# Optimization experiments

Hardware: AMD Instinct MI355X
Metric: run time of the kernel (lower is better)

Reference implementation:

```python
import jax, jax.numpy as jnp
import numpy as np
import math

N = 50000        # nodes
DEG = 16         # regular out-degree -> E = N*DEG edges, grouped by source node
B = 64           # graphs in batch
F = 128          # num_node_features
H = 128          # nhid == enhid
RATIO = 0.5      # edge_ratio
NUM_CONVS = 3
E = N * DEG


def setup_inputs() -> dict:
    key = jax.random.key(0)
    ks = jax.random.split(key, 18)
    s = 0.05
    x = jax.random.normal(ks[0], (N, F), jnp.float32)
    edge_src = jnp.repeat(jnp.arange(N, dtype=jnp.int32), DEG)          # sorted by src
    edge_dst = jax.random.randint(ks[1], (E,), 0, N, jnp.int32)
    batch = ((jnp.arange(N) * B) // N).astype(jnp.int32)                 # sorted graph ids
    edge_attr = jnp.ones((E, 1), jnp.float32)                            # edge_attr=None branch
    inp = {"x": x, "edge_attr": edge_attr, "edge_src": edge_src,
           "edge_dst": edge_dst, "batch": batch}
    # GCNConv weights: [F->H, H->H, H->H]
    inp["W_gcn0"] = jax.random.normal(ks[2], (F, H), jnp.float32) * s
    inp["b_gcn0"] = jnp.zeros((H,), jnp.float32)
    inp["W_gcn1"] = jax.random.normal(ks[3], (H, H), jnp.float32) * s
    inp["b_gcn1"] = jnp.zeros((H,), jnp.float32)
    inp["W_gcn2"] = jax.random.normal(ks[4], (H, H), jnp.float32) * s
    inp["b_gcn2"] = jnp.zeros((H,), jnp.float32)
    # EGNN edge convs: [1->H, H->H]
    inp["W_eg0"] = jax.random.normal(ks[5], (1, H), jnp.float32) * s
    inp["b_eg0"] = jnp.zeros((H,), jnp.float32)
    inp["W_eg1"] = jax.random.normal(ks[6], (H, H), jnp.float32) * s
    inp["b_eg1"] = jnp.zeros((H,), jnp.float32)
    # score convs: [H->1, H->1]
    inp["W_sc0"] = jax.random.normal(ks[7], (H, 1), jnp.float32) * s
    inp["b_sc0"] = jnp.zeros((1,), jnp.float32)
    inp["W_sc1"] = jax.random.normal(ks[8], (H, 1), jnp.float32) * s
    inp["b_sc1"] = jnp.zeros((1,), jnp.float32)
    return inp


def _gcn(x, src, dst, ew, W, b):
    # PyG GCNConv: add self-loops (weight 1), symmetric deg normalization, aggregate at dst.
    n = x.shape[0]
    loop = jnp.arange(n, dtype=src.dtype)
    src2 = jnp.concatenate([src, loop])
    dst2 = jnp.concatenate([dst, loop])
    ew2 = jnp.concatenate([ew, jnp.ones((n,), ew.dtype)])
    deg = jax.ops.segment_sum(ew2, dst2, n)
    dinv = jnp.where(deg > 0, jax.lax.rsqrt(jnp.maximum(deg, 1e-12)), 0.0)
    norm = dinv[src2] * dinv[dst2] * ew2                                  # [E+n]
    msg = (x @ W)[src2] * norm[:, None]                                    # gather + scale
    return jax.ops.segment_sum(msg, dst2, n) + b                           # scatter-add


def _egnn(e, src, W, b):
    # Edge conv: scatter edge features to their source node, gather back, linear map.
    agg = jax.ops.segment_sum(e, src, N)
    return agg[src] @ W + b


def _pool(h, batch):
    gmax = jax.ops.segment_max(h, batch, B)
    gsum = jax.ops.segment_sum(h, batch, B)
    cnt = jax.ops.segment_sum(jnp.ones((h.shape[0],), h.dtype), batch, B)
    gmean = gsum / cnt[:, None]
    return jnp.concatenate([gmax, gmean, gsum], axis=1)                    # [B, 3H]


def reference(x, edge_attr, edge_src, edge_dst, batch,
              W_gcn0, b_gcn0, W_gcn1, b_gcn1, W_gcn2, b_gcn2,
              W_eg0, b_eg0, W_eg1, b_eg1, W_sc0, b_sc0, W_sc1, b_sc1):
    gW = [W_gcn0, W_gcn1, W_gcn2]
    gb = [b_gcn0, b_gcn1, b_gcn2]
    eW = [W_eg0, W_eg1]
    eb = [b_eg0, b_eg1]
    sW = [W_sc0, W_sc1]
    sb = [b_sc0, b_sc1]
    src, dst = edge_src, edge_dst
    deg = DEG
    ew = jnp.ones((src.shape[0],), jnp.float32)
    h = x
    ea = edge_attr
    xs = jnp.zeros((B, 3 * H), jnp.float32)
    for i in range(NUM_CONVS):
        h = jax.nn.relu(_gcn(h, src, dst, ew, gW[i], gb[i]))
        if i < NUM_CONVS - 1:
            ea = jax.nn.relu(_egnn(ea, src, eW[i], eb[i]))
            score = jnp.tanh(_egnn(ea, src, sW[i], sb[i])[:, 0])           # [E_cur]
            k = math.ceil(RATIO * deg)                                      # per-src-node top-k
            vals, idx = jax.lax.top_k(score.reshape(N, deg), k)             # [N,k]
            dst = jnp.take_along_axis(dst.reshape(N, deg), idx, axis=1).reshape(-1)
            flat = (jnp.arange(N)[:, None] * deg + idx).reshape(-1)
            ea = ea[flat]
            src = jnp.repeat(jnp.arange(N, dtype=src.dtype), k)
            ew = jnp.clip(vals.reshape(-1), 0.0, 1.0)
            deg = k
        xs = xs + _pool(h, batch)
    return xs
```

## Files before the change

kernel.cpp:

```cpp
#include <hip/hip_runtime.h>
#include <math.h>

#define NNODES 50000
#define DEGREE 16
#define NGRAPH 64
#define CAP 64
#define LDA 136
#define NXCD 8
#define XRANGE (NNODES / NXCD)
#define NTILE 782
#define ACHUNK 784
#define BCAP 192

typedef unsigned short u16;
typedef unsigned int u32;
typedef unsigned long long u64;
using short8 = __attribute__((ext_vector_type(8))) short;
using f32x4  = __attribute__((ext_vector_type(4))) float;
using fv4    = __attribute__((ext_vector_type(4))) float;

__device__ __forceinline__ u16 f2bf(float f) {
  union { float f; u32 u; } v; v.f = f;
  u32 u = v.u;
  return (u16)((u + 0x7FFFu + ((u >> 16) & 1u)) >> 16);
}
__device__ __forceinline__ float2 bf2x2(u32 u) {
  union { u32 u; float f; } lo, hi;
  lo.u = (u & 0xFFFFu) << 16; hi.u = u & 0xFFFF0000u;
  return make_float2(lo.f, hi.f);
}
__device__ __forceinline__ u32 pack2(float x, float y) {
  return (u32)f2bf(x) | ((u32)f2bf(y) << 16);
}
__device__ __forceinline__ int lowerb(const int* b, int n, int v) {
  int lo = 0, hi = n;
  while (lo < hi) { int m = (lo + hi) >> 1; if (b[m] < v) lo = m + 1; else hi = m; }
  return lo;
}

__device__ __forceinline__ void cons8(uint4 v, float w, float* acc) {
  float2 p;
  p = bf2x2(v.x); acc[0] = fmaf(w, p.x, acc[0]); acc[1] = fmaf(w, p.y, acc[1]);
  p = bf2x2(v.y); acc[2] = fmaf(w, p.x, acc[2]); acc[3] = fmaf(w, p.y, acc[3]);
  p = bf2x2(v.z); acc[4] = fmaf(w, p.x, acc[4]); acc[5] = fmaf(w, p.y, acc[5]);
  p = bf2x2(v.w); acc[6] = fmaf(w, p.x, acc[6]); acc[7] = fmaf(w, p.y, acc[7]);
}
__device__ __forceinline__ void consP(uint4 v, float* mx, float* sm) {
  float2 p;
  p = bf2x2(v.x);
  mx[0] = fmaxf(mx[0], p.x); sm[0] += p.x; mx[1] = fmaxf(mx[1], p.y); sm[1] += p.y;
  p = bf2x2(v.y);
  mx[2] = fmaxf(mx[2], p.x); sm[2] += p.x; mx[3] = fmaxf(mx[3], p.y); sm[3] += p.y;
  p = bf2x2(v.z);
  mx[4] = fmaxf(mx[4], p.x); sm[4] += p.x; mx[5] = fmaxf(mx[5], p.y); sm[5] += p.y;
  p = bf2x2(v.w);
  mx[6] = fmaxf(mx[6], p.x); sm[6] += p.x; mx[7] = fmaxf(mx[7], p.y); sm[7] += p.y;
}

__global__ __launch_bounds__(256) void k_init(
    const float* __restrict__ eattr,
    const float* __restrict__ weg, const float* __restrict__ beg,
    const float* __restrict__ wsc, const float* __restrict__ bsc,
    const float* __restrict__ W0, const float* __restrict__ W1,
    const float* __restrict__ W2, const float* __restrict__ W3,
    float* __restrict__ ew1, float* __restrict__ agg0, u16* __restrict__ Wt,
    const int* __restrict__ edst, int* __restrict__ cnt,
    int* __restrict__ slots, int2* __restrict__ stag, int* __restrict__ scnt) {
  __shared__ int2 lbuf[NXCD * BCAP];
  __shared__ int lcnt[NXCD];
  int b = blockIdx.x, t = threadIdx.x;
  if (b < 196) {
    int i = b * 256 + t;
    if (i < NNODES) {
      const fv4* p = reinterpret_cast<const fv4*>(eattr + (size_t)i * DEGREE);
      float s = 0.f;
#pragma unroll
      for (int j = 0; j < 4; ++j) {
        fv4 w = __builtin_nontemporal_load(&p[j]);
        s += w.x + w.y + w.z + w.w;
      }
      agg0[i] = s;
      float sc = 0.f;
      for (int k = 0; k < 128; ++k) {
        float e = fmaxf(fmaf(s, weg[k], beg[k]), 0.f);
        sc = fmaf(e, wsc[k], sc);
      }
      float v1 = tanhf(fmaf(16.f, sc, bsc[0]));
      ew1[i] = fminf(fmaxf(v1, 0.f), 1.f);
    }
  } else if (b < 452) {
    int idx = (b - 196) * 256 + t;
    int which = idx >> 14, r = idx & 16383;
    int k = r >> 7, n = r & 127;
    const float* W = which == 0 ? W0 : which == 1 ? W1 : which == 2 ? W2 : W3;
    Wt[which * 16384 + n * 128 + k] = f2bf(W[k * 128 + n]);
  } else {
    int b2 = b - 452;
    if (t < NXCD) lcnt[t] = 0;
    __syncthreads();
    int e0 = b2 * ACHUNK;
    for (int k = 0; k < ACHUNK; k += 256) {
      int idx = k + t;
      int e = e0 + idx;
      if (idx < ACHUNK && e < NNODES * DEGREE) {
        int d = edst[e];
        u32 r = (u32)d / (u32)XRANGE;
        int pos = atomicAdd(&lcnt[r], 1);
        if (pos < BCAP) {
          lbuf[r * BCAP + pos] = make_int2(e, d);
        } else {
          int gp = atomicAdd(&cnt[d], 1);
          if (gp < CAP) slots[(size_t)d * CAP + gp] = e;
        }
      }
    }
    __syncthreads();
    for (int idx = t; idx < NXCD * BCAP; idx += 256) {
      int r = idx / BCAP, i = idx - r * BCAP;
      if (i < min(lcnt[r], BCAP))
        stag[((size_t)r * 1024 + b2) * BCAP + i] = lbuf[idx];
    }
    if (t < NXCD) scnt[t * 1024 + b2] = min(lcnt[t], BCAP);
  }
}

__global__ __launch_bounds__(256) void k_gemmF(
    int nFill, const int2* __restrict__ stag, const int* __restrict__ scnt,
    int* __restrict__ cnt, int* __restrict__ slots,
    int nGemm, const u16* __restrict__ A, const float* __restrict__ Af32,
    const u16* __restrict__ WtA, u16* __restrict__ outA,
    int nEg, const float* __restrict__ agg0, const float* __restrict__ weg,
    const float* __restrict__ beg, const u16* __restrict__ WtE,
    const float* __restrict__ beE, const float* __restrict__ wsc1,
    const float* __restrict__ bs1, float* __restrict__ ewOut) {
  __shared__ u16 Bs[128 * LDA];
  __shared__ u16 As[64 * LDA];
  int b = blockIdx.x, t = threadIdx.x;
  if (b < nFill) {
    int r = b & (NXCD - 1), sub = b >> 3;
    for (int q = 0; q < 8; ++q) {
      int sb = sub * 8 + q;
      int c = scnt[r * 1024 + sb];
      const int2* src = &stag[((size_t)r * 1024 + sb) * BCAP];
      for (int i = t; i < c; i += 256) {
        int2 v = src[i];
        int pos = atomicAdd(&cnt[v.y], 1);
        if (pos < CAP) slots[(size_t)v.y * CAP + pos] = v.x;
      }
    }
    return;
  }
  int bb = b - nFill;
  int eg = (bb >= nGemm);
  const u16* Wsrc = eg ? WtE : WtA;
  for (int i = t; i < 2048; i += 256) {
    int r = i >> 4, c = (i & 15) << 3;
    *reinterpret_cast<uint4*>(&Bs[r * LDA + c]) =
        *reinterpret_cast<const uint4*>(&Wsrc[r * 128 + c]);
  }
  int m0 = (eg ? (bb - nGemm) : bb) * 64;
  if (eg) {
    for (int idx = t; idx < 64 * 128; idx += 256) {
      int r = idx >> 7, k = idx & 127;
      int row = m0 + r;
      float a = (row < NNODES) ? agg0[row] : 0.f;
      float v = 8.f * fmaxf(fmaf(a, weg[k], beg[k]), 0.f);
      As[r * LDA + k] = f2bf(v);
    }
  } else if (Af32) {
    for (int i = t; i < 1024; i += 256) {
      int r = i >> 4, c = (i & 15) << 3;
      int row = m0 + r;
      uint4 o = make_uint4(0u, 0u, 0u, 0u);
      if (row < NNODES) {
        const fv4* px = reinterpret_cast<const fv4*>(Af32 + (size_t)row * 128 + c);
        fv4 v0 = __builtin_nontemporal_load(&px[0]);
        fv4 v1 = __builtin_nontemporal_load(&px[1]);
        o.x = pack2(v0.x, v0.y); o.y = pack2(v0.z, v0.w);
        o.z = pack2(v1.x, v1.y); o.w = pack2(v1.z, v1.w);
      }
      *reinterpret_cast<uint4*>(&As[r * LDA + c]) = o;
    }
  } else {
    for (int i = t; i < 1024; i += 256) {
      int r = i >> 4, c = (i & 15) << 3;
      int row = m0 + r;
      uint4 v = make_uint4(0u, 0u, 0u, 0u);
      if (row < NNODES) v = *reinterpret_cast<const uint4*>(&A[(size_t)row * 128 + c]);
      *reinterpret_cast<uint4*>(&As[r * LDA + c]) = v;
    }
  }
  __syncthreads();
  int wave = t >> 6, lane = t & 63;
  int lm = lane & 15, quad = lane >> 4;
  f32x4 z = {0.f, 0.f, 0.f, 0.f};
  f32x4 acc[8];
#pragma unroll
  for (int n = 0; n < 8; ++n) acc[n] = z;
  const u16* arow = &As[(wave * 16 + lm) * LDA + quad * 8];
#pragma unroll
  for (int kc = 0; kc < 4; ++kc) {
    short8 af = *reinterpret_cast<const short8*>(arow + kc * 32);
#pragma unroll
    for (int n = 0; n < 8; ++n) {
      short8 bf = *reinterpret_cast<const short8*>(
          &Bs[(n * 16 + lm) * LDA + kc * 32 + quad * 8]);
      acc[n] = __builtin_amdgcn_mfma_f32_16x16x32_bf16(af, bf, acc[n], 0, 0, 0);
    }
  }
  if (!eg) {
#pragma unroll
    for (int n = 0; n < 8; ++n) {
      int col = n * 16 + lm;
#pragma unroll
      for (int r = 0; r < 4; ++r) {
        int row = m0 + wave * 16 + quad * 4 + r;
        if (row < NNODES) outA[(size_t)row * 128 + col] = f2bf(acc[n][r]);
      }
    }
  } else {
    float s0 = 0.f, s1 = 0.f, s2 = 0.f, s3 = 0.f;
#pragma unroll
    for (int n = 0; n < 8; ++n) {
      int col = n * 16 + lm;
      float bb2 = beE[col], wv = wsc1[col];
      s0 = fmaf(fmaxf(acc[n][0] + bb2, 0.f), wv, s0);
      s1 = fmaf(fmaxf(acc[n][1] + bb2, 0.f), wv, s1);
      s2 = fmaf(fmaxf(acc[n][2] + bb2, 0.f), wv, s2);
      s3 = fmaf(fmaxf(acc[n][3] + bb2, 0.f), wv, s3);
    }
#pragma unroll
    for (int m = 8; m >= 1; m >>= 1) {
      s0 += __shfl_xor(s0, m, 64);
      s1 += __shfl_xor(s1, m, 64);
      s2 += __shfl_xor(s2, m, 64);
      s3 += __shfl_xor(s3, m, 64);
    }
    if (lm == 0) {
      float bsv = bs1[0];
      float sv[4] = {s0, s1, s2, s3};
#pragma unroll
      for (int r = 0; r < 4; ++r) {
        int row = m0 + wave * 16 + quad * 4 + r;
        if (row < NNODES) {
          float v = tanhf(fmaf(8.f, sv[r], bsv));
          ewOut[row] = fminf(fmaxf(v, 0.f), 1.f);
        }
      }
    }
  }
}

template <int MODE>
__global__ __launch_bounds__(256) void k_agg(
    int nAgg, const u16* __restrict__ xwb, const int* __restrict__ cnt,
    const int* __restrict__ slots, const float* __restrict__ wsrc,
    const float* __restrict__ dinv, const float* __restrict__ bias,
    u16* __restrict__ hout,
    const u16* __restrict__ hpool, const int* __restrict__ batch,
    float* __restrict__ out,
    const float* __restrict__ ew1g, float* __restrict__ dv1,
    float* __restrict__ ws1,
    const float* __restrict__ ew2g, float* __restrict__ dv2,
    float* __restrict__ ws2) {
  constexpr int keep = (MODE == 0) ? 16 : (MODE == 1) ? 8 : 4;
  constexpr bool L0 = (MODE == 0);
  constexpr int poolAdd = (MODE >= 2);
  __shared__ float P[1024];
  int b = blockIdx.x, t = threadIdx.x;
  int lane = t & 63;
  int q = lane >> 4, li = lane & 15;
  if (b < nAgg) {
    int n = (b * 256 + t) >> 6;
    if (n >= NNODES) return;
    int c = min(cnt[n], CAP);
    u32 e = 0;
    if (lane < c) e = (u32)slots[(size_t)n * CAP + lane];
    if (L0) {
      u32 j = e & 15u; int srcn = (int)(e >> 4);
      float e1 = 0.f, e2 = 0.f;
      if (lane < c && j < 8u) {
        e1 = ew1g[srcn];
        if (j < 4u) e2 = ew2g[srcn];
      }
#pragma unroll
      for (int m = 32; m >= 1; m >>= 1) {
        e1 += __shfl_xor(e1, m, 64);
        e2 += __shfl_xor(e2, m, 64);
      }
      if (lane == 0) {
        float d1 = rsqrtf(1.0f + e1), d2 = rsqrtf(1.0f + e2);
        dv1[n] = d1; ws1[n] = d1 * ew1g[n];
        dv2[n] = d2; ws2[n] = d2 * ew2g[n];
      }
    }
    int kc; u32 ce;
    if (keep < 16) {
      bool valid = (lane < c) && ((e & 15u) < (u32)keep);
      u64 mask = __ballot(valid);
      kc = (int)__popcll(mask);
      u64 lt = ((u64)1 << lane) - 1;
      int pos = valid ? (int)__popcll(mask & lt) : 63 - (int)__popcll((~mask) & lt);
      ce = (u32)__builtin_amdgcn_ds_permute(pos << 2, (int)e);
    } else { kc = c; ce = e; }
    int sl = 0; float wl = 0.f;
    if (lane < kc) {
      sl = (int)(ce >> 4);
      wl = L0 ? rsqrtf(1.0f + (float)min(cnt[sl], CAP)) : wsrc[sl];
    }
    const uint4* b4 = reinterpret_cast<const uint4*>(xwb);
    uint4 selfv = b4[n * 16 + li];
    float acc[8] = {0.f, 0.f, 0.f, 0.f, 0.f, 0.f, 0.f, 0.f};
    for (int i = 0; i < kc; i += 16) {
      int r0 = i + q, r1 = i + 4 + q, r2 = i + 8 + q, r3 = i + 12 + q;
      int s0 = __shfl(sl, r0, 64); float w0 = __shfl(wl, r0, 64);
      int s1 = __shfl(sl, r1, 64); float w1 = __shfl(wl, r1, 64);
      int s2 = __shfl(sl, r2, 64); float w2 = __shfl(wl, r2, 64);
      int s3 = __shfl(sl, r3, 64); float w3 = __shfl(wl, r3, 64);
      if (r0 >= kc) { s0 = n; w0 = 0.f; }
      if (r1 >= kc) { s1 = n; w1 = 0.f; }
      if (r2 >= kc) { s2 = n; w2 = 0.f; }
      if (r3 >= kc) { s3 = n; w3 = 0.f; }
      uint4 v0 = b4[s0 * 16 + li];
      uint4 v1 = selfv, v2 = selfv, v3 = selfv;
      if (i + 4 < kc)  v1 = b4[s1 * 16 + li];
      if (i + 8 < kc)  v2 = b4[s2 * 16 + li];
      if (i + 12 < kc) v3 = b4[s3 * 16 + li];
      cons8(v0, w0, acc);
      cons8(v1, w1, acc);
      cons8(v2, w2, acc);
      cons8(v3, w3, acc);
    }
#pragma unroll
    for (int k = 0; k < 8; ++k) {
      acc[k] += __shfl_xor(acc[k], 16, 64);
      acc[k] += __shfl_xor(acc[k], 32, 64);
    }
    float di = L0 ? rsqrtf(1.0f + (float)c) : dinv[n];
    float dd = di * di;
    const f32x4* bp = reinterpret_cast<const f32x4*>(bias);
    f32x4 bv0 = bp[li * 2], bv1 = bp[li * 2 + 1];
    float2 p0 = bf2x2(selfv.x), p1 = bf2x2(selfv.y),
           p2 = bf2x2(selfv.z), p3 = bf2x2(selfv.w);
    float r0 = fmaxf(fmaf(di, acc[0], fmaf(dd, p0.x, bv0.x)), 0.f);
    float r1 = fmaxf(fmaf(di, acc[1], fmaf(dd, p0.y, bv0.y)), 0.f);
    float r2 = fmaxf(fmaf(di, acc[2], fmaf(dd, p1.x, bv0.z)), 0.f);
    float r3 = fmaxf(fmaf(di, acc[3], fmaf(dd, p1.y, bv0.w)), 0.f);
    float r4 = fmaxf(fmaf(di, acc[4], fmaf(dd, p2.x, bv1.x)), 0.f);
    float r5 = fmaxf(fmaf(di, acc[5], fmaf(dd, p2.y, bv1.y)), 0.f);
    float r6 = fmaxf(fmaf(di, acc[6], fmaf(dd, p3.x, bv1.z)), 0.f);
    float r7 = fmaxf(fmaf(di, acc[7], fmaf(dd, p3.y, bv1.w)), 0.f);
    if (q == 0) {
      uint4 o;
      o.x = pack2(r0, r1); o.y = pack2(r2, r3);
      o.z = pack2(r4, r5); o.w = pack2(r6, r7);
      reinterpret_cast<uint4*>(hout + (size_t)n * 128)[li] = o;
    }
  } else {
    int g = b - nAgg;
    int wv = t >> 6;
    int lo = lowerb(batch, NNODES, g);
    int hi = lowerb(batch, NNODES, g + 1);
    const uint4* hb4 = reinterpret_cast<const uint4*>(hpool);
    float mx[8] = {0.f, 0.f, 0.f, 0.f, 0.f, 0.f, 0.f, 0.f};
    float sm[8] = {0.f, 0.f, 0.f, 0.f, 0.f, 0.f, 0.f, 0.f};
    int n = lo + wv * 4 + q;
    for (; n + 48 < hi; n += 64) {
      uint4 v0 = hb4[(size_t)n * 16 + li];
      uint4 v1 = hb4[(size_t)(n + 16) * 16 + li];
      uint4 v2 = hb4[(size_t)(n + 32) * 16 + li];
      uint4 v3 = hb4[(size_t)(n + 48) * 16 + li];
      consP(v0, mx, sm); consP(v1, mx, sm);
      consP(v2, mx, sm); consP(v3, mx, sm);
    }
    for (; n < hi; n += 16) {
      uint4 v = hb4[(size_t)n * 16 + li];
      consP(v, mx, sm);
    }
#pragma unroll
    for (int k = 0; k < 8; ++k) {
      mx[k] = fmaxf(mx[k], __shfl_xor(mx[k], 16, 64));
      mx[k] = fmaxf(mx[k], __shfl_xor(mx[k], 32, 64));
      sm[k] += __shfl_xor(sm[k], 16, 64);
      sm[k] += __shfl_xor(sm[k], 32, 64);
    }
    if (q == 0) {
#pragma unroll
      for (int k = 0; k < 8; ++k) {
        P[(wv * 16 + li) * 16 + k] = mx[k];
        P[(wv * 16 + li) * 16 + 8 + k] = sm[k];
      }
    }
    __syncthreads();
    if (t < 128) {
      int li2 = t >> 3, k = t & 7;
      int o0 = li2 * 16 + k, o1 = o0 + 8;
      float m = fmaxf(fmaxf(P[o0], P[256 + o0]),
                      fmaxf(P[512 + o0], P[768 + o0]));
      float s = P[o1] + P[256 + o1] + P[512 + o1] + P[768 + o1];
      float cf = (float)(hi - lo);
      int col = li2 * 8 + k;
      float* og = out + g * 384;
      if (poolAdd) {
        og[col] += m; og[128 + col] += s / cf; og[256 + col] += s;
      } else {
        og[col] = m;  og[128 + col] = s / cf;  og[256 + col] = s;
      }
    }
  }
}

extern "C" void kernel_launch(void* const* d_in, const int* in_sizes, int n_in,
                              void* d_out, int out_size, void* d_ws, size_t ws_size,
                              hipStream_t stream) {
  const float* x     = (const float*)d_in[0];
  const float* eattr = (const float*)d_in[1];
  const int*   edst  = (const int*)d_in[3];
  const int*   batch = (const int*)d_in[4];
  const float* Wg0 = (const float*)d_in[5];  const float* bg0 = (const float*)d_in[6];
  const float* Wg1 = (const float*)d_in[7];  const float* bg1 = (const float*)d_in[8];
  const float* Wg2 = (const float*)d_in[9];  const float* bg2 = (const float*)d_in[10];
  const float* We0 = (const float*)d_in[11]; const float* be0 = (const float*)d_in[12];
  const float* We1 = (const float*)d_in[13]; const float* be1 = (const float*)d_in[14];
  const float* Ws0 = (const float*)d_in[15]; const float* bs0 = (const float*)d_in[16];
  const float* Ws1 = (const float*)d_in[17]; const float* bs1 = (const float*)d_in[18];
  float* out = (float*)d_out;

  char* ws = (char*)d_ws;
  const size_t NBH = (size_t)NNODES * 128 * 2;
  size_t off = 0;
  auto alloc = [&](size_t bytes) { void* p = ws + off; off = (off + bytes + 255) & ~(size_t)255; return p; };
  u16*   XWb   = (u16*)alloc(NBH);
  u16*   Hb0   = (u16*)alloc(NBH);
  u16*   Hb1   = (u16*)alloc(NBH);
  u16*   Hb2   = (u16*)alloc(NBH);
  u16*   Wtb   = (u16*)alloc(4 * 128 * 128 * 2);
  int*   slots = (int*)alloc((size_t)NNODES * CAP * 4);
  int*   cnt   = (int*)alloc((size_t)NNODES * 4);
  int2*  stag  = (int2*)alloc((size_t)NXCD * 1024 * BCAP * 8);
  int*   scnt  = (int*)alloc((size_t)NXCD * 1024 * 4);
  float* agg0  = (float*)alloc((size_t)NNODES * 4);
  float* ew1   = (float*)alloc((size_t)NNODES * 4);
  float* ew2   = (float*)alloc((size_t)NNODES * 4);
  float* dinv1 = (float*)alloc((size_t)NNODES * 4);
  float* wsrc1 = (float*)alloc((size_t)NNODES * 4);
  float* dinv2 = (float*)alloc((size_t)NNODES * 4);
  float* wsrc2 = (float*)alloc((size_t)NNODES * 4);

  hipMemsetAsync(cnt, 0, (size_t)NNODES * 4, stream);
  k_init<<<1476, 256, 0, stream>>>(eattr, We0, be0, Ws0, bs0,
                                   Wg0, Wg1, Wg2, We1, ew1, agg0, Wtb,
                                   edst, cnt, slots, stag, scnt);
  k_gemmF<<<1024 + 2 * NTILE, 256, 0, stream>>>(
      1024, stag, scnt, cnt, slots,
      NTILE, nullptr, x, Wtb, XWb,
      NTILE, agg0, We0, be0, Wtb + 3 * 16384, be1, Ws1, bs1, ew2);
  k_agg<0><<<12500, 256, 0, stream>>>(12500, XWb, cnt, slots, nullptr, nullptr,
                                      bg0, Hb0, nullptr, batch, nullptr,
                                      ew1, dinv1, wsrc1, ew2, dinv2, wsrc2);
  k_gemmF<<<NTILE, 256, 0, stream>>>(
      0, nullptr, nullptr, nullptr, nullptr,
      NTILE, Hb0, nullptr, Wtb + 16384, XWb,
      0, nullptr, nullptr, nullptr, nullptr, nullptr, nullptr, nullptr, nullptr);
  k_agg<1><<<12500 + NGRAPH, 256, 0, stream>>>(12500, XWb, cnt, slots, wsrc1,
                                               dinv1, bg1, Hb1, Hb0, batch, out,
                                               nullptr, nullptr, nullptr,
                                               nullptr, nullptr, nullptr);
  k_gemmF<<<NTILE, 256, 0, stream>>>(
      0, nullptr, nullptr, nullptr, nullptr,
      NTILE, Hb1, nullptr, Wtb + 2 * 16384, XWb,
      0, nullptr, nullptr, nullptr, nullptr, nullptr, nullptr, nullptr, nullptr);
  k_agg<2><<<12500 + NGRAPH, 256, 0, stream>>>(12500, XWb, cnt, slots, wsrc2,
                                               dinv2, bg2, Hb2, Hb1, batch, out,
                                               nullptr, nullptr, nullptr,
                                               nullptr, nullptr, nullptr);
  k_agg<3><<<NGRAPH, 256, 0, stream>>>(0, nullptr, cnt, slots, nullptr, nullptr,
                                       nullptr, nullptr, Hb2, batch, out,
                                       nullptr, nullptr, nullptr,
                                       nullptr, nullptr, nullptr);
}
```

Before: 319.6 us.

## Load GEMM A-fragments directly into registers and schedule GEMM blocks before fill

```diff
diff --git a/kernel.cpp b/kernel.cpp
--- a/kernel.cpp
+++ b/kernel.cpp
@@ -134,10 +134,11 @@
     const float* __restrict__ beE, const float* __restrict__ wsc1,
     const float* __restrict__ bs1, float* __restrict__ ewOut) {
   __shared__ u16 Bs[128 * LDA];
-  __shared__ u16 As[64 * LDA];
   int b = blockIdx.x, t = threadIdx.x;
-  if (b < nFill) {
-    int r = b & (NXCD - 1), sub = b >> 3;
+  int nWork = nGemm + nEg;
+  if (b >= nWork) {
+    int f = b - nWork;
+    int r = f & (NXCD - 1), sub = f >> 3;
     for (int q = 0; q < 8; ++q) {
       int sb = sub * 8 + q;
       int c = scnt[r * 1024 + sb];
@@ -150,62 +151,74 @@
     }
     return;
   }
-  int bb = b - nFill;
-  int eg = (bb >= nGemm);
+  int eg = (b >= nGemm);
   const u16* Wsrc = eg ? WtE : WtA;
   for (int i = t; i < 2048; i += 256) {
     int r = i >> 4, c = (i & 15) << 3;
     *reinterpret_cast<uint4*>(&Bs[r * LDA + c]) =
         *reinterpret_cast<const uint4*>(&Wsrc[r * 128 + c]);
   }
-  int m0 = (eg ? (bb - nGemm) : bb) * 64;
+  int m0 = (eg ? (b - nGemm) : b) * 64;
+  int wave = t >> 6, lane = t & 63;
+  int lm = lane & 15, quad = lane >> 4;
+  int row = m0 + wave * 16 + lm;
+  short8 af[4];
   if (eg) {
-    for (int idx = t; idx < 64 * 128; idx += 256) {
-      int r = idx >> 7, k = idx & 127;
-      int row = m0 + r;
-      float a = (row < NNODES) ? agg0[row] : 0.f;
-      float v = 8.f * fmaxf(fmaf(a, weg[k], beg[k]), 0.f);
-      As[r * LDA + k] = f2bf(v);
+    float a = (row < NNODES) ? agg0[row] : 0.f;
+#pragma unroll
+    for (int kc = 0; kc < 4; ++kc) {
+      int k0 = kc * 32 + quad * 8;
+      float v[8];
+#pragma unroll
+      for (int j = 0; j < 8; ++j)
+        v[j] = 8.f * fmaxf(fmaf(a, weg[k0 + j], beg[k0 + j]), 0.f);
+      uint4 o;
+      o.x = pack2(v[0], v[1]); o.y = pack2(v[2], v[3]);
+      o.z = pack2(v[4], v[5]); o.w = pack2(v[6], v[7]);
+      af[kc] = *reinterpret_cast<short8*>(&o);
     }
   } else if (Af32) {
-    for (int i = t; i < 1024; i += 256) {
-      int r = i >> 4, c = (i & 15) << 3;
-      int row = m0 + r;
-      uint4 o = make_uint4(0u, 0u, 0u, 0u);
-      if (row < NNODES) {
-        const fv4* px = reinterpret_cast<const fv4*>(Af32 + (size_t)row * 128 + c);
-        fv4 v0 = __builtin_nontemporal_load(&px[0]);
-        fv4 v1 = __builtin_nontemporal_load(&px[1]);
+    if (row < NNODES) {
+      const fv4* px = reinterpret_cast<const fv4*>(Af32 + (size_t)row * 128);
+#pragma unroll
+      for (int kc = 0; kc < 4; ++kc) {
+        int k0 = (kc * 32 + quad * 8) >> 2;
+        fv4 v0 = __builtin_nontemporal_load(&px[k0]);
+        fv4 v1 = __builtin_nontemporal_load(&px[k0 + 1]);
+        uint4 o;
         o.x = pack2(v0.x, v0.y); o.y = pack2(v0.z, v0.w);
         o.z = pack2(v1.x, v1.y); o.w = pack2(v1.z, v1.w);
-      }
-      *reinterpret_cast<uint4*>(&As[r * LDA + c]) = o;
+        af[kc] = *reinterpret_cast<short8*>(&o);
+      }
+    } else {
+      uint4 o = make_uint4(0u, 0u, 0u, 0u);
+#pragma unroll
+      for (int kc = 0; kc < 4; ++kc) af[kc] = *reinterpret_cast<short8*>(&o);
     }
   } else {
-    for (int i = t; i < 1024; i += 256) {
-      int r = i >> 4, c = (i & 15) << 3;
-      int row = m0 + r;
-      uint4 v = make_uint4(0u, 0u, 0u, 0u);
-      if (row < NNODES) v = *reinterpret_cast<const uint4*>(&A[(size_t)row * 128 + c]);
-      *reinterpret_cast<uint4*>(&As[r * LDA + c]) = v;
+    if (row < NNODES) {
+#pragma unroll
+      for (int kc = 0; kc < 4; ++kc)
+        af[kc] = *reinterpret_cast<const short8*>(
+            &A[(size_t)row * 128 + kc * 32 + quad * 8]);
+    } else {
+      uint4 o = make_uint4(0u, 0u, 0u, 0u);
+#pragma unroll
+      for (int kc = 0; kc < 4; ++kc) af[kc] = *reinterpret_cast<short8*>(&o);
     }
   }
   __syncthreads();
-  int wave = t >> 6, lane = t & 63;
-  int lm = lane & 15, quad = lane >> 4;
   f32x4 z = {0.f, 0.f, 0.f, 0.f};
   f32x4 acc[8];
 #pragma unroll
   for (int n = 0; n < 8; ++n) acc[n] = z;
-  const u16* arow = &As[(wave * 16 + lm) * LDA + quad * 8];
 #pragma unroll
   for (int kc = 0; kc < 4; ++kc) {
-    short8 af = *reinterpret_cast<const short8*>(arow + kc * 32);
 #pragma unroll
     for (int n = 0; n < 8; ++n) {
       short8 bf = *reinterpret_cast<const short8*>(
           &Bs[(n * 16 + lm) * LDA + kc * 32 + quad * 8]);
-      acc[n] = __builtin_amdgcn_mfma_f32_16x16x32_bf16(af, bf, acc[n], 0, 0, 0);
+      acc[n] = __builtin_amdgcn_mfma_f32_16x16x32_bf16(af[kc], bf, acc[n], 0, 0, 0);
     }
   }
   if (!eg) {
@@ -214,8 +227,8 @@
       int col = n * 16 + lm;
 #pragma unroll
       for (int r = 0; r < 4; ++r) {
-        int row = m0 + wave * 16 + quad * 4 + r;
-        if (row < NNODES) outA[(size_t)row * 128 + col] = f2bf(acc[n][r]);
+        int orow = m0 + wave * 16 + quad * 4 + r;
+        if (orow < NNODES) outA[(size_t)orow * 128 + col] = f2bf(acc[n][r]);
       }
     }
   } else {
@@ -241,10 +254,10 @@
       float sv[4] = {s0, s1, s2, s3};
 #pragma unroll
       for (int r = 0; r < 4; ++r) {
-        int row = m0 + wave * 16 + quad * 4 + r;
-        if (row < NNODES) {
+        int orow = m0 + wave * 16 + quad * 4 + r;
+        if (orow < NNODES) {
           float v = tanhf(fmaf(8.f, sv[r], bsv));
-          ewOut[row] = fminf(fmaxf(v, 0.f), 1.f);
+          ewOut[orow] = fminf(fmaxf(v, 0.f), 1.f);
         }
       }
     }
@@ -451,7 +464,7 @@
   k_init<<<1476, 256, 0, stream>>>(eattr, We0, be0, Ws0, bs0,
                                    Wg0, Wg1, Wg2, We1, ew1, agg0, Wtb,
                                    edst, cnt, slots, stag, scnt);
-  k_gemmF<<<1024 + 2 * NTILE, 256, 0, stream>>>(
+  k_gemmF<<<2 * NTILE + 1024, 256, 0, stream>>>(
       1024, stag, scnt, cnt, slots,
       NTILE, nullptr, x, Wtb, XWb,
       NTILE, agg0, We0, be0, Wtb + 3 * 16384, be1, Ws1, bs1, ew2);
```

Result: faster. 303.1 us (-5.2%).
